# Optimization experiments

Measured on AMD Instinct MI355X. Metric: run time of the kernel, lower is better.

Reference implementation:

```python
import jax, jax.numpy as jnp
import numpy as np

B, N, D, U = 8, 2048, 512, 128


def setup_inputs() -> dict:
    key = jax.random.key(0)
    k_x, k_q, k_k, k_v, k_o = jax.random.split(key, 5)
    scale_in = 1.0 / np.sqrt(D)
    scale_u = 1.0 / np.sqrt(U)
    return {
        "inputs": jax.random.normal(k_x, (B, N, D), dtype=jnp.float32),
        "W_q": jax.random.normal(k_q, (D, U), dtype=jnp.float32) * scale_in,
        "W_k": jax.random.normal(k_k, (D, U), dtype=jnp.float32) * scale_in,
        "W_v": jax.random.normal(k_v, (D, U), dtype=jnp.float32) * scale_in,
        "W_o": jax.random.normal(k_o, (U, D), dtype=jnp.float32) * scale_u,
        "b_o": jnp.zeros((D,), dtype=jnp.float32),
    }


def reference(inputs, W_q, W_k, W_v, W_o, b_o):
    # Single-head scaled dot-product self-attention + output dense + residual
    Q = jnp.einsum('bnd,du->bnu', inputs, W_q)
    K = jnp.einsum('bnd,du->bnu', inputs, W_k)
    V = jnp.einsum('bnd,du->bnu', inputs, W_v)
    inv_sqrt_u = 1.0 / jnp.sqrt(jnp.asarray(W_q.shape[-1], inputs.dtype))
    scores = jnp.einsum('bnu,bmu->bnm', Q, K) * inv_sqrt_u  # [B,N,N]
    attn = jax.nn.softmax(scores, axis=-1)
    ctx = jnp.einsum('bnm,bmu->bnu', attn, V)  # [B,N,U]
    return jnp.einsum('bnu,ud->bnd', ctx, W_o) + b_o + inputs
```

## Files before the change

kernel.cpp:

```cpp
#include <hip/hip_runtime.h>

#define BB 8
#define NN 2048
#define DD 512
#define UU 128
#define SPLITS 4
#define KSPLIT 512

typedef __bf16 bf16_t;
typedef __bf16 bf16x4 __attribute__((ext_vector_type(4)));
typedef __bf16 bf16x8 __attribute__((ext_vector_type(8)));
typedef float floatx4 __attribute__((ext_vector_type(4)));

__device__ __forceinline__ floatx4 mfma16(bf16x8 a, bf16x8 b, floatx4 c) {
  return __builtin_amdgcn_mfma_f32_16x16x32_bf16(a, b, c, 0, 0, 0);
}

#define SW(r, g) ((((g) ^ ((r) & 7)) * 8))

__global__ __launch_bounds__(256) void cast_x_kernel(const float* __restrict__ x,
                                                     bf16_t* __restrict__ xb) {
  int gid = blockIdx.x * 256 + threadIdx.x;
  float4 v = reinterpret_cast<const float4*>(x)[gid];
  bf16x4 o;
  o[0] = (bf16_t)v.x; o[1] = (bf16_t)v.y; o[2] = (bf16_t)v.z; o[3] = (bf16_t)v.w;
  reinterpret_cast<bf16x4*>(xb)[gid] = o;
}

__global__ __launch_bounds__(256) void pack_w_kernel(const float* __restrict__ wq,
                                                     const float* __restrict__ wk,
                                                     const float* __restrict__ wv,
                                                     const float* __restrict__ wo,
                                                     bf16_t* __restrict__ wqkvt,
                                                     bf16_t* __restrict__ wot) {
  int gid = blockIdx.x * 256 + threadIdx.x;
  if (gid < 384 * 512) {
    int nrow = gid >> 9;
    int k = gid & 511;
    const float* src = (nrow < 128) ? wq : ((nrow < 256) ? wk : wv);
    int n = nrow & 127;
    wqkvt[gid] = (bf16_t)src[k * 128 + n];
  } else {
    int g = gid - 384 * 512;
    int nrow = g >> 7;
    int k = g & 127;
    wot[g] = (bf16_t)wo[k * 512 + nrow];
  }
}

__global__ __launch_bounds__(256) void qkv_gemm_kernel(const bf16_t* __restrict__ xb,
                                                       const bf16_t* __restrict__ wqkvt,
                                                       bf16_t* __restrict__ Q,
                                                       bf16_t* __restrict__ K,
                                                       bf16_t* __restrict__ Vt) {
  __shared__ bf16_t lA[64 * 64];
  __shared__ bf16_t lB[64 * 64];
  const int m0 = blockIdx.x * 64;
  const int n0 = blockIdx.y * 64;
  const int tid = threadIdx.x;
  const int w = tid >> 6, lane = tid & 63;
  const int quad = lane >> 4, l15 = lane & 15;

  floatx4 zero4 = {0.f, 0.f, 0.f, 0.f};
  floatx4 acc[4];
#pragma unroll
  for (int nt = 0; nt < 4; nt++) acc[nt] = zero4;

  for (int kc = 0; kc < 512; kc += 64) {
    __syncthreads();
    for (int t = tid; t < 512; t += 256) {
      int r = t >> 3, g = t & 7;
      *reinterpret_cast<bf16x8*>(&lA[r * 64 + SW(r, g)]) =
          *reinterpret_cast<const bf16x8*>(&xb[(size_t)(m0 + r) * 512 + kc + g * 8]);
      *reinterpret_cast<bf16x8*>(&lB[r * 64 + SW(r, g)]) =
          *reinterpret_cast<const bf16x8*>(&wqkvt[(size_t)(n0 + r) * 512 + kc + g * 8]);
    }
    __syncthreads();
#pragma unroll
    for (int kb = 0; kb < 2; kb++) {
      bf16x8 a = *reinterpret_cast<const bf16x8*>(&lA[(w * 16 + l15) * 64 + SW(l15, kb * 4 + quad)]);
#pragma unroll
      for (int nt = 0; nt < 4; nt++) {
        bf16x8 b = *reinterpret_cast<const bf16x8*>(&lB[(nt * 16 + l15) * 64 + SW(l15, kb * 4 + quad)]);
        acc[nt] = mfma16(a, b, acc[nt]);
      }
    }
  }

#pragma unroll
  for (int nt = 0; nt < 4; nt++) {
    int n = n0 + nt * 16 + l15;
#pragma unroll
    for (int r = 0; r < 4; r++) {
      int token = m0 + w * 16 + quad * 4 + r;
      bf16_t h = (bf16_t)acc[nt][r];
      if (n < 128) {
        Q[(size_t)token * 128 + n] = h;
      } else if (n < 256) {
        K[(size_t)token * 128 + (n - 128)] = h;
      } else {
        int b = token >> 11;
        int t = token & 2047;
        Vt[((size_t)b * 128 + (n - 256)) * 2048 + t] = h;
      }
    }
  }
}

__global__ __launch_bounds__(256, 2) void attn_kernel(const bf16_t* __restrict__ Q,
                                                      const bf16_t* __restrict__ K,
                                                      const bf16_t* __restrict__ Vt,
                                                      bf16_t* __restrict__ Op,
                                                      float* __restrict__ ml) {
  __shared__ bf16_t lK[64 * 128];
  __shared__ bf16_t lV[128 * 64];
  __shared__ bf16_t lP[4][32 * 64];

  const int b = blockIdx.y;
  const int qb = blockIdx.x;
  const int s = blockIdx.z;
  const int tid = threadIdx.x;
  const int w = tid >> 6, lane = tid & 63;
  const int quad = lane >> 4, l15 = lane & 15;
  const float c = 0.08838834764831845f * 1.4426950408889634f;

  bf16x8 qf[2][4];
#pragma unroll
  for (int mt = 0; mt < 2; mt++) {
    const bf16_t* qrow =
        &Q[((size_t)b * NN + qb * 128 + w * 32 + mt * 16 + l15) * 128 + quad * 8];
#pragma unroll
    for (int kb = 0; kb < 4; kb++)
      qf[mt][kb] = *reinterpret_cast<const bf16x8*>(qrow + kb * 32);
  }

  float l_part[2] = {0.f, 0.f};
  floatx4 zero4 = {0.f, 0.f, 0.f, 0.f};
  floatx4 accO[2][8];
#pragma unroll
  for (int mt = 0; mt < 2; mt++)
#pragma unroll
    for (int ut = 0; ut < 8; ut++) accO[mt][ut] = zero4;

  bf16_t* pw = &lP[w][0];
  const int kt0 = s * KSPLIT;
  for (int kt = kt0; kt < kt0 + KSPLIT; kt += 64) {
    __syncthreads();
    for (int t = tid; t < 1024; t += 256) {
      int r = t >> 4, g = t & 15;
      *reinterpret_cast<bf16x8*>(&lK[r * 128 + SW(r, g)]) =
          *reinterpret_cast<const bf16x8*>(&K[((size_t)b * NN + kt + r) * 128 + g * 8]);
    }
    for (int t = tid; t < 1024; t += 256) {
      int r = t >> 3, g = t & 7;
      *reinterpret_cast<bf16x8*>(&lV[r * 64 + SW(r, g)]) =
          *reinterpret_cast<const bf16x8*>(&Vt[((size_t)b * 128 + r) * 2048 + kt + g * 8]);
    }
    __syncthreads();

    floatx4 accS[4][2];
#pragma unroll
    for (int km = 0; km < 4; km++)
#pragma unroll
      for (int mt = 0; mt < 2; mt++) accS[km][mt] = zero4;
#pragma unroll
    for (int kb = 0; kb < 4; kb++) {
#pragma unroll
      for (int km = 0; km < 4; km++) {
        bf16x8 kf = *reinterpret_cast<const bf16x8*>(
            &lK[(km * 16 + l15) * 128 + SW(l15, kb * 4 + quad)]);
#pragma unroll
        for (int mt = 0; mt < 2; mt++)
          accS[km][mt] = mfma16(kf, qf[mt][kb], accS[km][mt]);
      }
    }

#pragma unroll
    for (int km = 0; km < 4; km++) {
#pragma unroll
      for (int mt = 0; mt < 2; mt++) {
        float p0 = __builtin_amdgcn_exp2f(accS[km][mt][0] * c);
        float p1 = __builtin_amdgcn_exp2f(accS[km][mt][1] * c);
        float p2 = __builtin_amdgcn_exp2f(accS[km][mt][2] * c);
        float p3 = __builtin_amdgcn_exp2f(accS[km][mt][3] * c);
        l_part[mt] += (p0 + p1) + (p2 + p3);
        bf16x4 pk;
        pk[0] = (bf16_t)p0; pk[1] = (bf16_t)p1; pk[2] = (bf16_t)p2; pk[3] = (bf16_t)p3;
        int row = mt * 16 + l15;
        int g = km * 2 + (quad >> 1);
        *reinterpret_cast<bf16x4*>(
            &pw[row * 64 + ((g ^ (row & 7)) * 8) + (quad & 1) * 4]) = pk;
      }
    }
    asm volatile("s_waitcnt lgkmcnt(0)" ::: "memory");

#pragma unroll
    for (int kb = 0; kb < 2; kb++) {
      bf16x8 pa[2];
#pragma unroll
      for (int mt = 0; mt < 2; mt++)
        pa[mt] = *reinterpret_cast<const bf16x8*>(
            &pw[(mt * 16 + l15) * 64 + SW(l15, kb * 4 + quad)]);
#pragma unroll
      for (int ut = 0; ut < 8; ut++) {
        bf16x8 bv = *reinterpret_cast<const bf16x8*>(
            &lV[(ut * 16 + l15) * 64 + SW(l15, kb * 4 + quad)]);
#pragma unroll
        for (int mt = 0; mt < 2; mt++)
          accO[mt][ut] = mfma16(pa[mt], bv, accO[mt][ut]);
      }
    }
  }

#pragma unroll
  for (int mt = 0; mt < 2; mt++) {
    float v = l_part[mt];
    v += __shfl_xor(v, 16);
    v += __shfl_xor(v, 32);
    l_part[mt] = v;
  }

  size_t base = ((size_t)(b * 16 + qb) * SPLITS + s);
  bf16_t* op = Op + base * (128 * 128);
  float* mlp = ml + base * 128;
#pragma unroll
  for (int mt = 0; mt < 2; mt++)
#pragma unroll
    for (int ut = 0; ut < 8; ut++)
#pragma unroll
      for (int r = 0; r < 4; r++)
        op[(w * 32 + mt * 16 + quad * 4 + r) * 128 + ut * 16 + l15] =
            (bf16_t)accO[mt][ut][r];
  if (quad == 0) {
#pragma unroll
    for (int mt = 0; mt < 2; mt++) mlp[w * 32 + mt * 16 + l15] = l_part[mt];
  }
}

__global__ __launch_bounds__(256) void merge_kernel(const bf16_t* __restrict__ Op,
                                                    const float* __restrict__ ml,
                                                    bf16_t* __restrict__ ctx) {
  const int blk = blockIdx.x;
  const int q = threadIdx.x >> 1;
  const int u0 = (threadIdx.x & 1) * 64;

  float L = 0.f;
  float o[64];
#pragma unroll
  for (int j = 0; j < 64; j++) o[j] = 0.f;
#pragma unroll
  for (int s = 0; s < SPLITS; s++) {
    L += ml[((size_t)blk * SPLITS + s) * 128 + q];
    const bf16_t* op = Op + ((size_t)blk * SPLITS + s) * 16384 + q * 128 + u0;
#pragma unroll
    for (int v = 0; v < 8; v++) {
      bf16x8 ch = *reinterpret_cast<const bf16x8*>(op + v * 8);
#pragma unroll
      for (int j = 0; j < 8; j++) o[v * 8 + j] += (float)ch[j];
    }
  }
  float inv = 1.0f / L;
  const int bb = blk >> 4, qbl = blk & 15;
  bf16_t* dst = ctx + ((size_t)bb * NN + qbl * 128 + q) * 128 + u0;
#pragma unroll
  for (int v = 0; v < 8; v++) {
    bf16x8 ch;
#pragma unroll
    for (int j = 0; j < 8; j++) ch[j] = (bf16_t)(o[v * 8 + j] * inv);
    *reinterpret_cast<bf16x8*>(dst + v * 8) = ch;
  }
}

__global__ __launch_bounds__(256) void out_gemm_kernel(const bf16_t* __restrict__ ctx,
                                                       const bf16_t* __restrict__ wot,
                                                       const float* __restrict__ bo,
                                                       const float* __restrict__ x0,
                                                       float* __restrict__ out) {
  __shared__ bf16_t lA[64 * 128];
  __shared__ bf16_t lB[64 * 128];
  const int m0 = blockIdx.x * 64;
  const int n0 = blockIdx.y * 64;
  const int tid = threadIdx.x;
  const int w = tid >> 6, lane = tid & 63;
  const int quad = lane >> 4, l15 = lane & 15;

  for (int t = tid; t < 1024; t += 256) {
    int r = t >> 4, g = t & 15;
    *reinterpret_cast<bf16x8*>(&lA[r * 128 + SW(r, g)]) =
        *reinterpret_cast<const bf16x8*>(&ctx[(size_t)(m0 + r) * 128 + g * 8]);
    *reinterpret_cast<bf16x8*>(&lB[r * 128 + SW(r, g)]) =
        *reinterpret_cast<const bf16x8*>(&wot[(size_t)(n0 + r) * 128 + g * 8]);
  }
  __syncthreads();

  floatx4 zero4 = {0.f, 0.f, 0.f, 0.f};
  floatx4 acc[4];
#pragma unroll
  for (int nt = 0; nt < 4; nt++) acc[nt] = zero4;
#pragma unroll
  for (int kb = 0; kb < 4; kb++) {
    bf16x8 a = *reinterpret_cast<const bf16x8*>(&lA[(w * 16 + l15) * 128 + SW(l15, kb * 4 + quad)]);
#pragma unroll
    for (int nt = 0; nt < 4; nt++) {
      bf16x8 bfr = *reinterpret_cast<const bf16x8*>(&lB[(nt * 16 + l15) * 128 + SW(l15, kb * 4 + quad)]);
      acc[nt] = mfma16(a, bfr, acc[nt]);
    }
  }

#pragma unroll
  for (int nt = 0; nt < 4; nt++) {
    int n = n0 + nt * 16 + l15;
    float bias = bo[n];
#pragma unroll
    for (int r = 0; r < 4; r++) {
      size_t m = m0 + w * 16 + quad * 4 + r;
      out[m * 512 + n] = acc[nt][r] + bias + x0[m * 512 + n];
    }
  }
}

extern "C" void kernel_launch(void* const* d_in, const int* in_sizes, int n_in,
                              void* d_out, int out_size, void* d_ws, size_t ws_size,
                              hipStream_t stream) {
  const float* x  = (const float*)d_in[0];
  const float* wq = (const float*)d_in[1];
  const float* wk = (const float*)d_in[2];
  const float* wv = (const float*)d_in[3];
  const float* wo = (const float*)d_in[4];
  const float* bo = (const float*)d_in[5];
  float* out = (float*)d_out;

  char* ws = (char*)d_ws;
  bf16_t* Qb    = (bf16_t*)(ws);
  bf16_t* Kb    = (bf16_t*)(ws + 4194304);
  bf16_t* Vt    = (bf16_t*)(ws + 2 * 4194304);
  bf16_t* Ctx   = (bf16_t*)(ws + 3 * 4194304);
  bf16_t* Wqkvt = (bf16_t*)(ws + 4 * 4194304);
  bf16_t* Wot   = (bf16_t*)(ws + 4 * 4194304 + 393216);
  bf16_t* Xb    = (bf16_t*)(ws + 4 * 4194304 + 524288);
  bf16_t* Op    = (bf16_t*)(ws + 4 * 4194304 + 524288);
  float*  ml    = (float*)(ws + 4 * 4194304 + 524288 + 16777216);

  cast_x_kernel<<<8192, 256, 0, stream>>>(x, Xb);
  pack_w_kernel<<<1024, 256, 0, stream>>>(wq, wk, wv, wo, Wqkvt, Wot);
  qkv_gemm_kernel<<<dim3(256, 6), 256, 0, stream>>>(Xb, Wqkvt, Qb, Kb, Vt);
  attn_kernel<<<dim3(16, 8, SPLITS), 256, 0, stream>>>(Qb, Kb, Vt, Op, ml);
  merge_kernel<<<128, 256, 0, stream>>>(Op, ml, Ctx);
  out_gemm_kernel<<<dim3(256, 8), 256, 0, stream>>>(Ctx, Wot, bo, x, out);
}
```

Baseline: 173.8 us.

## Use direct global-to-LDS loads with pre-swizzled layouts and double attention splits

```diff
diff --git a/kernel.cpp b/kernel.cpp
--- a/kernel.cpp
+++ b/kernel.cpp
@@ -4,8 +4,8 @@
 #define NN 2048
 #define DD 512
 #define UU 128
-#define SPLITS 4
-#define KSPLIT 512
+#define SPLITS 8
+#define KSPLIT 256
 
 typedef __bf16 bf16_t;
 typedef __bf16 bf16x4 __attribute__((ext_vector_type(4)));
@@ -18,13 +18,24 @@
 
 #define SW(r, g) ((((g) ^ ((r) & 7)) * 8))
 
+__device__ __forceinline__ void gld_lds16(const bf16_t* g, bf16_t* l) {
+  __builtin_amdgcn_global_load_lds(
+      (const __attribute__((address_space(1))) unsigned int*)g,
+      (__attribute__((address_space(3))) unsigned int*)l, 16, 0, 0);
+}
+
 __global__ __launch_bounds__(256) void cast_x_kernel(const float* __restrict__ x,
                                                      bf16_t* __restrict__ xb) {
-  int gid = blockIdx.x * 256 + threadIdx.x;
-  float4 v = reinterpret_cast<const float4*>(x)[gid];
-  bf16x4 o;
-  o[0] = (bf16_t)v.x; o[1] = (bf16_t)v.y; o[2] = (bf16_t)v.z; o[3] = (bf16_t)v.w;
-  reinterpret_cast<bf16x4*>(xb)[gid] = o;
+  int G = blockIdx.x * 256 + threadIdx.x;
+  int token = G >> 6;
+  int g = G & 63;
+  int dstg = (g & 56) | ((g & 7) ^ (token & 7));
+  const float4* src = reinterpret_cast<const float4*>(x) + (size_t)G * 2;
+  float4 a = src[0], b = src[1];
+  bf16x8 o;
+  o[0] = (bf16_t)a.x; o[1] = (bf16_t)a.y; o[2] = (bf16_t)a.z; o[3] = (bf16_t)a.w;
+  o[4] = (bf16_t)b.x; o[5] = (bf16_t)b.y; o[6] = (bf16_t)b.z; o[7] = (bf16_t)b.w;
+  *reinterpret_cast<bf16x8*>(&xb[(size_t)token * 512 + dstg * 8]) = o;
 }
 
 __global__ __launch_bounds__(256) void pack_w_kernel(const float* __restrict__ wq,
@@ -36,23 +47,25 @@
   int gid = blockIdx.x * 256 + threadIdx.x;
   if (gid < 384 * 512) {
     int nrow = gid >> 9;
-    int k = gid & 511;
+    int kdst = gid & 511;
+    int ksrc = (kdst & ~56) | (((((kdst >> 3) & 7)) ^ (nrow & 7)) << 3);
     const float* src = (nrow < 128) ? wq : ((nrow < 256) ? wk : wv);
     int n = nrow & 127;
-    wqkvt[gid] = (bf16_t)src[k * 128 + n];
+    wqkvt[gid] = (bf16_t)src[ksrc * 128 + n];
   } else {
     int g = gid - 384 * 512;
     int nrow = g >> 7;
-    int k = g & 127;
-    wot[g] = (bf16_t)wo[k * 512 + nrow];
-  }
-}
-
-__global__ __launch_bounds__(256) void qkv_gemm_kernel(const bf16_t* __restrict__ xb,
-                                                       const bf16_t* __restrict__ wqkvt,
-                                                       bf16_t* __restrict__ Q,
-                                                       bf16_t* __restrict__ K,
-                                                       bf16_t* __restrict__ Vt) {
+    int kdst = g & 127;
+    int ksrc = (kdst & ~56) | (((((kdst >> 3) & 7)) ^ (nrow & 7)) << 3);
+    wot[g] = (bf16_t)wo[ksrc * 512 + nrow];
+  }
+}
+
+__global__ __launch_bounds__(256, 4) void qkv_gemm_kernel(const bf16_t* __restrict__ xb,
+                                                          const bf16_t* __restrict__ wqkvt,
+                                                          bf16_t* __restrict__ Q,
+                                                          bf16_t* __restrict__ K,
+                                                          bf16_t* __restrict__ Vt) {
   __shared__ bf16_t lA[64 * 64];
   __shared__ bf16_t lB[64 * 64];
   const int m0 = blockIdx.x * 64;
@@ -68,13 +81,14 @@
 
   for (int kc = 0; kc < 512; kc += 64) {
     __syncthreads();
-    for (int t = tid; t < 512; t += 256) {
+#pragma unroll
+    for (int i = 0; i < 2; i++) {
+      int t = tid + i * 256;
       int r = t >> 3, g = t & 7;
-      *reinterpret_cast<bf16x8*>(&lA[r * 64 + SW(r, g)]) =
-          *reinterpret_cast<const bf16x8*>(&xb[(size_t)(m0 + r) * 512 + kc + g * 8]);
-      *reinterpret_cast<bf16x8*>(&lB[r * 64 + SW(r, g)]) =
-          *reinterpret_cast<const bf16x8*>(&wqkvt[(size_t)(n0 + r) * 512 + kc + g * 8]);
-    }
+      gld_lds16(&xb[(size_t)(m0 + r) * 512 + kc + g * 8], &lA[t * 8]);
+      gld_lds16(&wqkvt[(size_t)(n0 + r) * 512 + kc + g * 8], &lB[t * 8]);
+    }
+    asm volatile("s_waitcnt vmcnt(0)" ::: "memory");
     __syncthreads();
 #pragma unroll
     for (int kb = 0; kb < 2; kb++) {
@@ -97,17 +111,21 @@
       if (n < 128) {
         Q[(size_t)token * 128 + n] = h;
       } else if (n < 256) {
-        K[(size_t)token * 128 + (n - 128)] = h;
+        int nk = n - 128;
+        int nsw = (nk & ~56) | ((((nk >> 3) & 7) ^ (token & 7)) << 3);
+        K[(size_t)token * 128 + nsw] = h;
       } else {
         int b = token >> 11;
         int t = token & 2047;
-        Vt[((size_t)b * 128 + (n - 256)) * 2048 + t] = h;
-      }
-    }
-  }
-}
-
-__global__ __launch_bounds__(256, 2) void attn_kernel(const bf16_t* __restrict__ Q,
+        int u = n - 256;
+        int tsw = (t & ~56) | ((((t >> 3) & 7) ^ (u & 7)) << 3);
+        Vt[((size_t)b * 128 + u) * 2048 + tsw] = h;
+      }
+    }
+  }
+}
+
+__global__ __launch_bounds__(256, 3) void attn_kernel(const bf16_t* __restrict__ Q,
                                                       const bf16_t* __restrict__ K,
                                                       const bf16_t* __restrict__ Vt,
                                                       bf16_t* __restrict__ Op,
@@ -146,16 +164,22 @@
   const int kt0 = s * KSPLIT;
   for (int kt = kt0; kt < kt0 + KSPLIT; kt += 64) {
     __syncthreads();
-    for (int t = tid; t < 1024; t += 256) {
-      int r = t >> 4, g = t & 15;
-      *reinterpret_cast<bf16x8*>(&lK[r * 128 + SW(r, g)]) =
-          *reinterpret_cast<const bf16x8*>(&K[((size_t)b * NN + kt + r) * 128 + g * 8]);
-    }
-    for (int t = tid; t < 1024; t += 256) {
-      int r = t >> 3, g = t & 7;
-      *reinterpret_cast<bf16x8*>(&lV[r * 64 + SW(r, g)]) =
-          *reinterpret_cast<const bf16x8*>(&Vt[((size_t)b * 128 + r) * 2048 + kt + g * 8]);
-    }
+    {
+      const bf16_t* ksrc = &K[((size_t)b * NN + kt) * 128];
+#pragma unroll
+      for (int i = 0; i < 4; i++) {
+        int t = tid + i * 256;
+        gld_lds16(ksrc + (size_t)t * 8, &lK[t * 8]);
+      }
+      const bf16_t* vbase = &Vt[(size_t)b * 128 * 2048 + kt];
+#pragma unroll
+      for (int i = 0; i < 4; i++) {
+        int t = tid + i * 256;
+        int r = t >> 3, g = t & 7;
+        gld_lds16(vbase + (size_t)r * 2048 + g * 8, &lV[t * 8]);
+      }
+    }
+    asm volatile("s_waitcnt vmcnt(0)" ::: "memory");
     __syncthreads();
 
     floatx4 accS[4][2];
@@ -242,18 +266,18 @@
                                                     bf16_t* __restrict__ ctx) {
   const int blk = blockIdx.x;
   const int q = threadIdx.x >> 1;
-  const int u0 = (threadIdx.x & 1) * 64;
+  const int u0 = blockIdx.y * 64 + (threadIdx.x & 1) * 32;
 
   float L = 0.f;
-  float o[64];
-#pragma unroll
-  for (int j = 0; j < 64; j++) o[j] = 0.f;
+  float o[32];
+#pragma unroll
+  for (int j = 0; j < 32; j++) o[j] = 0.f;
 #pragma unroll
   for (int s = 0; s < SPLITS; s++) {
     L += ml[((size_t)blk * SPLITS + s) * 128 + q];
     const bf16_t* op = Op + ((size_t)blk * SPLITS + s) * 16384 + q * 128 + u0;
 #pragma unroll
-    for (int v = 0; v < 8; v++) {
+    for (int v = 0; v < 4; v++) {
       bf16x8 ch = *reinterpret_cast<const bf16x8*>(op + v * 8);
 #pragma unroll
       for (int j = 0; j < 8; j++) o[v * 8 + j] += (float)ch[j];
@@ -261,21 +285,23 @@
   }
   float inv = 1.0f / L;
   const int bb = blk >> 4, qbl = blk & 15;
-  bf16_t* dst = ctx + ((size_t)bb * NN + qbl * 128 + q) * 128 + u0;
-#pragma unroll
-  for (int v = 0; v < 8; v++) {
+  bf16_t* dst = ctx + ((size_t)bb * NN + qbl * 128 + q) * 128;
+#pragma unroll
+  for (int v = 0; v < 4; v++) {
+    int g = (u0 >> 3) + v;
+    int gsw = (g & 8) | ((g & 7) ^ (q & 7));
     bf16x8 ch;
 #pragma unroll
     for (int j = 0; j < 8; j++) ch[j] = (bf16_t)(o[v * 8 + j] * inv);
-    *reinterpret_cast<bf16x8*>(dst + v * 8) = ch;
-  }
-}
-
-__global__ __launch_bounds__(256) void out_gemm_kernel(const bf16_t* __restrict__ ctx,
-                                                       const bf16_t* __restrict__ wot,
-                                                       const float* __restrict__ bo,
-                                                       const float* __restrict__ x0,
-                                                       float* __restrict__ out) {
+    *reinterpret_cast<bf16x8*>(dst + gsw * 8) = ch;
+  }
+}
+
+__global__ __launch_bounds__(256, 4) void out_gemm_kernel(const bf16_t* __restrict__ ctx,
+                                                          const bf16_t* __restrict__ wot,
+                                                          const float* __restrict__ bo,
+                                                          const float* __restrict__ x0,
+                                                          float* __restrict__ out) {
   __shared__ bf16_t lA[64 * 128];
   __shared__ bf16_t lB[64 * 128];
   const int m0 = blockIdx.x * 64;
@@ -284,13 +310,13 @@
   const int w = tid >> 6, lane = tid & 63;
   const int quad = lane >> 4, l15 = lane & 15;
 
-  for (int t = tid; t < 1024; t += 256) {
-    int r = t >> 4, g = t & 15;
-    *reinterpret_cast<bf16x8*>(&lA[r * 128 + SW(r, g)]) =
-        *reinterpret_cast<const bf16x8*>(&ctx[(size_t)(m0 + r) * 128 + g * 8]);
-    *reinterpret_cast<bf16x8*>(&lB[r * 128 + SW(r, g)]) =
-        *reinterpret_cast<const bf16x8*>(&wot[(size_t)(n0 + r) * 128 + g * 8]);
-  }
+#pragma unroll
+  for (int i = 0; i < 4; i++) {
+    int t = tid + i * 256;
+    gld_lds16(&ctx[(size_t)m0 * 128 + t * 8], &lA[t * 8]);
+    gld_lds16(&wot[(size_t)n0 * 128 + t * 8], &lB[t * 8]);
+  }
+  asm volatile("s_waitcnt vmcnt(0)" ::: "memory");
   __syncthreads();
 
   floatx4 zero4 = {0.f, 0.f, 0.f, 0.f};
@@ -339,12 +365,12 @@
   bf16_t* Wot   = (bf16_t*)(ws + 4 * 4194304 + 393216);
   bf16_t* Xb    = (bf16_t*)(ws + 4 * 4194304 + 524288);
   bf16_t* Op    = (bf16_t*)(ws + 4 * 4194304 + 524288);
-  float*  ml    = (float*)(ws + 4 * 4194304 + 524288 + 16777216);
-
-  cast_x_kernel<<<8192, 256, 0, stream>>>(x, Xb);
+  float*  ml    = (float*)(ws + 4 * 4194304 + 524288 + 33554432);
+
+  cast_x_kernel<<<4096, 256, 0, stream>>>(x, Xb);
   pack_w_kernel<<<1024, 256, 0, stream>>>(wq, wk, wv, wo, Wqkvt, Wot);
   qkv_gemm_kernel<<<dim3(256, 6), 256, 0, stream>>>(Xb, Wqkvt, Qb, Kb, Vt);
   attn_kernel<<<dim3(16, 8, SPLITS), 256, 0, stream>>>(Qb, Kb, Vt, Op, ml);
-  merge_kernel<<<128, 256, 0, stream>>>(Op, ml, Ctx);
+  merge_kernel<<<dim3(128, 2), 256, 0, stream>>>(Op, ml, Ctx);
   out_gemm_kernel<<<dim3(256, 8), 256, 0, stream>>>(Ctx, Wot, bo, x, out);
 }
```

Result: faster. 162.4 us (-6.6%).
